# Optimization experiments

Measured on AMD Instinct MI355X. Metric: run time of the kernel, lower is better.

The kernel has to match this reference:

```python
import jax, jax.numpy as jnp
import numpy as np

# Static graph structure: gene nodes first, GO-term nodes last (mask is sorted).
N_GENE, N_GOID = 40000, 10000
N = N_GENE + N_GOID
E = 800000
INPUT_DIM, H1, H2, OUT_DIM, GOID_DIM = 1280, 256, 128, 64, 4096


def setup_inputs() -> dict:
    key = jax.random.key(0)
    ks = jax.random.split(key, 16)
    s = 0.02
    return {
        "x": jax.random.normal(ks[0], (N, GOID_DIM), jnp.float32),
        "edge_index": jax.random.randint(ks[1], (2, E), 0, N),
        "mask": jnp.concatenate([jnp.ones(N_GENE, bool), jnp.zeros(N_GOID, bool)]),
        # goid_dnn: Linear(4096,1024) -> ReLU -> Linear(1024,INPUT_DIM) -> ReLU
        "Wd1": jax.random.normal(ks[2], (GOID_DIM, 1024), jnp.float32) * s,
        "bd1": jnp.zeros((1024,), jnp.float32),
        "Wd2": jax.random.normal(ks[3], (1024, INPUT_DIM), jnp.float32) * s,
        "bd2": jnp.zeros((INPUT_DIM,), jnp.float32),
        # GCNConv layers
        "W1": jax.random.normal(ks[4], (INPUT_DIM, H1), jnp.float32) * s,
        "b1": jnp.zeros((H1,), jnp.float32),
        "W2": jax.random.normal(ks[5], (H1, H2), jnp.float32) * s,
        "b2": jnp.zeros((H2,), jnp.float32),
        # goid projections
        "Wp1": jax.random.normal(ks[6], (INPUT_DIM, H1), jnp.float32) * s,
        "bp1": jnp.zeros((H1,), jnp.float32),
        "Wp2": jax.random.normal(ks[7], (H1, H2), jnp.float32) * s,
        "bp2": jnp.zeros((H2,), jnp.float32),
        # final fc
        "Wf": jax.random.normal(ks[8], (H2, OUT_DIM), jnp.float32) * s,
        "bf": jnp.zeros((OUT_DIM,), jnp.float32),
    }


def gcn_conv(x, W, b, src, dst):
    """PyG GCNConv: xW, then sym-normalized (A + I) aggregation, then bias."""
    # degree over targets with self-loops already appended to (src, dst)
    deg = jax.ops.segment_sum(jnp.ones_like(dst, x.dtype), dst, num_segments=N)
    dinv = jnp.where(deg > 0, jax.lax.rsqrt(deg), 0.0)
    norm = dinv[src] * dinv[dst]                       # [E+N]
    xw = x @ W                                          # [N, F_out]
    msg = xw[src] * norm[:, None]                       # gather-scale, [E+N, F_out]
    return jax.ops.segment_sum(msg, dst, num_segments=N) + b


def reference(x, edge_index, mask, Wd1, bd1, Wd2, bd2, W1, b1, W2, b2,
              Wp1, bp1, Wp2, bp2, Wf, bf):
    del mask  # structurally: first N_GENE rows are genes, rest are GO terms
    loop = jnp.arange(N, dtype=edge_index.dtype)
    src = jnp.concatenate([edge_index[0], loop])
    dst = jnp.concatenate([edge_index[1], loop])

    gene_x = x[:N_GENE, :INPUT_DIM]
    goid_x = x[N_GENE:]
    # goid_dnn runs under torch.no_grad() -> stop_gradient
    goid_t = jax.lax.stop_gradient(
        jax.nn.relu(jax.nn.relu(goid_x @ Wd1 + bd1) @ Wd2 + bd2))

    x_t = jnp.concatenate([gene_x, goid_t], axis=0)      # [N, INPUT_DIM]
    h1 = jax.nn.relu(gcn_conv(x_t, W1, b1, src, dst))    # dropout disabled (eval)
    p1 = goid_t @ Wp1 + bp1                              # goid_proj1
    h1 = h1.at[N_GENE:].set(p1)                          # masked scatter assign
    h2 = jax.nn.relu(gcn_conv(h1, W2, b2, src, dst))
    h2 = h2.at[N_GENE:].set(p1 @ Wp2 + bp2)              # goid_proj2(goid_proj1(...))
    return h2 @ Wf + bf                                  # [N, OUT_DIM]
```

## Files before the change

kernel.cpp:

```cpp
#include <hip/hip_runtime.h>

constexpr int kNGene = 40000;
constexpr int kNGoid = 10000;
constexpr int kN     = 50000;
constexpr int kE     = 800000;
constexpr int kInDim = 1280;
constexpr int kH1    = 256;
constexpr int kH2    = 128;
constexpr int kOut   = 64;
constexpr int kGDim  = 4096;
constexpr int kD1    = 1024;

typedef short bf16x8 __attribute__((ext_vector_type(8)));
typedef float f32x4  __attribute__((ext_vector_type(4)));

static __device__ __forceinline__ short f2bf(float f) {
  union { float f; unsigned u; } v; v.f = f;
  unsigned r = v.u + 0x7FFF + ((v.u >> 16) & 1);
  return (short)(r >> 16);
}
static __device__ __forceinline__ float bf2f(short s) {
  union { unsigned u; float f; } v;
  v.u = ((unsigned)(unsigned short)s) << 16;
  return v.f;
}
static __device__ __forceinline__ void gld16(const void* g, void* l) {
  __builtin_amdgcn_global_load_lds(
      (const __attribute__((address_space(1))) void*)g,
      (__attribute__((address_space(3))) void*)l, 16, 0, 0);
}

__global__ __launch_bounds__(256)
void k_cvt_rows(const float* __restrict__ src, int lda, short* __restrict__ dst,
                int rows, int cols) {
  int chunks_per_row = cols >> 3;
  long long total = (long long)rows * chunks_per_row;
  long long stride = (long long)gridDim.x * blockDim.x;
  for (long long i = blockIdx.x * (long long)blockDim.x + threadIdx.x; i < total; i += stride) {
    int r = (int)(i / chunks_per_row);
    int c = (int)(i - (long long)r * chunks_per_row) << 3;
    const float* sp = src + (size_t)r * lda + c;
    float4 v0 = *reinterpret_cast<const float4*>(sp);
    float4 v1 = *reinterpret_cast<const float4*>(sp + 4);
    bf16x8 t;
    t[0]=f2bf(v0.x); t[1]=f2bf(v0.y); t[2]=f2bf(v0.z); t[3]=f2bf(v0.w);
    t[4]=f2bf(v1.x); t[5]=f2bf(v1.y); t[6]=f2bf(v1.z); t[7]=f2bf(v1.w);
    *reinterpret_cast<bf16x8*>(dst + (size_t)r * cols + c) = t;
  }
}

__global__ void k_init(float* deg, int* gcount) {
  int i = blockIdx.x * blockDim.x + threadIdx.x;
  if (i < kN) deg[i] = 1.0f;
  if (i == 0) *gcount = 0;
}
__global__ void k_deg_hist(const int* __restrict__ ei, float* __restrict__ deg) {
  int e = blockIdx.x * blockDim.x + threadIdx.x;
  if (e < kE) atomicAdd(&deg[ei[kE + e]], 1.0f);
}
__global__ void k_rowassign(const float* __restrict__ deg, int* __restrict__ rowstart,
                            int* __restrict__ cursor, int* __restrict__ gcount) {
  int i = blockIdx.x * blockDim.x + threadIdx.x;
  int lane = threadIdx.x & 63;
  int c = (i < kNGene) ? ((int)deg[i] - 1) : 0;
  int incl = c;
#pragma unroll
  for (int off = 1; off < 64; off <<= 1) {
    int t = __shfl_up(incl, off, 64);
    if (lane >= off) incl += t;
  }
  int total = __shfl(incl, 63, 64);
  int base = 0;
  if (lane == 63) base = atomicAdd(gcount, total);
  base = __shfl(base, 63, 64);
  if (i < kNGene) {
    int s = base + incl - c;
    rowstart[i] = s;
    cursor[i] = s;
  }
}
__global__ void k_fill(const int* __restrict__ ei, const float* __restrict__ deg,
                       int* __restrict__ cursor, int2* __restrict__ edges) {
  int e = blockIdx.x * blockDim.x + threadIdx.x;
  if (e >= kE) return;
  int dst = ei[kE + e];
  if (dst >= kNGene) return;
  int src = ei[e];
  int pos = atomicAdd(&cursor[dst], 1);
  float nrm = rsqrtf(deg[src] * deg[dst]);
  edges[pos] = make_int2(src, __float_as_int(nrm));
}

template <int F, int OBF>
__global__ __launch_bounds__(256)
void k_gather_bf(const short* __restrict__ xw, const float* __restrict__ deg,
                 const int* __restrict__ rowstart, const int2* __restrict__ edges,
                 const float* __restrict__ bias, void* __restrict__ hv) {
  constexpr int VEC = F / 64;
  int row = (blockIdx.x * blockDim.x + threadIdx.x) >> 6;
  int lane = threadIdx.x & 63;
  if (row >= kNGene) return;
  float dg = deg[row];
  float inv = 1.0f / dg;
  float acc[VEC];
  {
    const short* xr = xw + (size_t)row * F + lane * VEC;
    if constexpr (VEC == 4) {
      short4 s = *reinterpret_cast<const short4*>(xr);
      acc[0] = bf2f(s.x) * inv; acc[1] = bf2f(s.y) * inv;
      acc[2] = bf2f(s.z) * inv; acc[3] = bf2f(s.w) * inv;
    } else {
      short2 s = *reinterpret_cast<const short2*>(xr);
      acc[0] = bf2f(s.x) * inv; acc[1] = bf2f(s.y) * inv;
    }
  }
  const int2* ep = edges + rowstart[row];
  int n = (int)dg - 1;
  int e = 0;
  for (; e + 1 < n; e += 2) {
    int2 p0 = ep[e], p1 = ep[e + 1];
    float n0 = __int_as_float(p0.y), n1 = __int_as_float(p1.y);
    const short* x0 = xw + (size_t)p0.x * F + lane * VEC;
    const short* x1 = xw + (size_t)p1.x * F + lane * VEC;
    if constexpr (VEC == 4) {
      short4 s0 = *reinterpret_cast<const short4*>(x0);
      short4 s1 = *reinterpret_cast<const short4*>(x1);
      acc[0] += bf2f(s0.x) * n0; acc[1] += bf2f(s0.y) * n0;
      acc[2] += bf2f(s0.z) * n0; acc[3] += bf2f(s0.w) * n0;
      acc[0] += bf2f(s1.x) * n1; acc[1] += bf2f(s1.y) * n1;
      acc[2] += bf2f(s1.z) * n1; acc[3] += bf2f(s1.w) * n1;
    } else {
      short2 s0 = *reinterpret_cast<const short2*>(x0);
      short2 s1 = *reinterpret_cast<const short2*>(x1);
      acc[0] += bf2f(s0.x) * n0; acc[1] += bf2f(s0.y) * n0;
      acc[0] += bf2f(s1.x) * n1; acc[1] += bf2f(s1.y) * n1;
    }
  }
  if (e < n) {
    int2 p0 = ep[e];
    float n0 = __int_as_float(p0.y);
    const short* x0 = xw + (size_t)p0.x * F + lane * VEC;
    if constexpr (VEC == 4) {
      short4 s0 = *reinterpret_cast<const short4*>(x0);
      acc[0] += bf2f(s0.x) * n0; acc[1] += bf2f(s0.y) * n0;
      acc[2] += bf2f(s0.z) * n0; acc[3] += bf2f(s0.w) * n0;
    } else {
      short2 s0 = *reinterpret_cast<const short2*>(x0);
      acc[0] += bf2f(s0.x) * n0; acc[1] += bf2f(s0.y) * n0;
    }
  }
#pragma unroll
  for (int v = 0; v < VEC; ++v) acc[v] = fmaxf(acc[v] + bias[lane * VEC + v], 0.f);
  if constexpr (OBF) {
    short* hp = (short*)hv + (size_t)row * F + lane * VEC;
    if constexpr (VEC == 4) {
      short4 o; o.x = f2bf(acc[0]); o.y = f2bf(acc[1]); o.z = f2bf(acc[2]); o.w = f2bf(acc[3]);
      *reinterpret_cast<short4*>(hp) = o;
    } else {
      short2 o; o.x = f2bf(acc[0]); o.y = f2bf(acc[1]);
      *reinterpret_cast<short2*>(hp) = o;
    }
  } else {
    float* hp = (float*)hv + (size_t)row * F + lane * VEC;
    if constexpr (VEC == 4) {
      float4 o; o.x = acc[0]; o.y = acc[1]; o.z = acc[2]; o.w = acc[3];
      *reinterpret_cast<float4*>(hp) = o;
    } else {
      float2 o; o.x = acc[0]; o.y = acc[1];
      *reinterpret_cast<float2*>(hp) = o;
    }
  }
}

__global__ __launch_bounds__(256)
void k_wtrans_all(const float* __restrict__ Wd1, short* __restrict__ Wd1t,
                  const float* __restrict__ Wd2, short* __restrict__ Wd2t,
                  const float* __restrict__ W1,  short* __restrict__ W1t,
                  const float* __restrict__ Wp1, short* __restrict__ Wp1t,
                  const float* __restrict__ W2,  short* __restrict__ W2t,
                  const float* __restrict__ Wp2, short* __restrict__ Wp2t) {
  __shared__ float t[32][33];
  int b = blockIdx.x;
  const float* W; short* Wt; int K, N, bi;
  if (b < 4096)      { W = Wd1; Wt = Wd1t; K = 4096; N = 1024; bi = b; }
  else if (b < 5376) { W = Wd2; Wt = Wd2t; K = 1024; N = 1280; bi = b - 4096; }
  else if (b < 5696) { W = W1;  Wt = W1t;  K = 1280; N = 256;  bi = b - 5376; }
  else if (b < 6016) { W = Wp1; Wt = Wp1t; K = 1280; N = 256;  bi = b - 5696; }
  else if (b < 6048) { W = W2;  Wt = W2t;  K = 256;  N = 128;  bi = b - 6016; }
  else               { W = Wp2; Wt = Wp2t; K = 256;  N = 128;  bi = b - 6048; }
  int nbx = N >> 5;
  int n0 = (bi % nbx) * 32, k0 = (bi / nbx) * 32;
  int tx = threadIdx.x & 31, ty = threadIdx.x >> 5;
#pragma unroll
  for (int p = 0; p < 4; ++p)
    t[ty + 8 * p][tx] = W[(size_t)(k0 + ty + 8 * p) * N + n0 + tx];
  __syncthreads();
#pragma unroll
  for (int p = 0; p < 4; ++p)
    Wt[(size_t)(n0 + ty + 8 * p) * K + k0 + tx] = f2bf(t[tx][ty + 8 * p]);
}

template <int RELU, int OBF>
__global__ __launch_bounds__(256)
void k_gemm_bf16a(const short* __restrict__ A, int lda,
                  const short* __restrict__ Bt,
                  const float* __restrict__ bias,
                  void* __restrict__ Cv, int ldc,
                  int M, int K)
{
  __shared__ __align__(16) short As[2][128 * 32];
  __shared__ __align__(16) short Bs[2][128 * 32];
  const int tid  = threadIdx.x;
  const int lane = tid & 63;
  const int wid  = tid >> 6;
  const int wr = wid >> 1, wc = wid & 1;
  const int row0 = blockIdx.y * 128;
  const int col0 = blockIdx.x * 128;
  const int l15 = lane & 15, l4 = lane >> 4;
  const int srow = lane >> 2, schunk = lane & 3;

  f32x4 acc[4][4] = {};

  auto stage = [&](int buf, int k0) {
#pragma unroll
    for (int q = 0; q < 2; ++q) {
      int seg = wid * 2 + q;
      int r = seg * 16 + srow;
      int grow = row0 + r;
      if (grow >= M) grow = M - 1;
      gld16(A + (size_t)grow * lda + k0 + schunk * 8, &As[buf][seg * 512]);
      int gcol = col0 + r;
      gld16(Bt + (size_t)gcol * K + k0 + schunk * 8, &Bs[buf][seg * 512]);
    }
  };

  stage(0, 0);
  __syncthreads();
  int cur = 0;
  for (int k0 = 0; k0 < K; k0 += 32) {
    if (k0 + 32 < K) stage(cur ^ 1, k0 + 32);
    bf16x8 af[4], bfr[4];
#pragma unroll
    for (int m = 0; m < 4; ++m)
      af[m] = *reinterpret_cast<bf16x8*>(&As[cur][(wr * 64 + m * 16 + l15) * 32 + l4 * 8]);
#pragma unroll
    for (int n = 0; n < 4; ++n)
      bfr[n] = *reinterpret_cast<bf16x8*>(&Bs[cur][(wc * 64 + n * 16 + l15) * 32 + l4 * 8]);
#pragma unroll
    for (int m = 0; m < 4; ++m)
#pragma unroll
      for (int n = 0; n < 4; ++n)
        acc[m][n] = __builtin_amdgcn_mfma_f32_16x16x32_bf16(af[m], bfr[n], acc[m][n], 0, 0, 0);
    __syncthreads();
    cur ^= 1;
  }

#pragma unroll
  for (int n = 0; n < 4; ++n) {
    int col = col0 + wc * 64 + n * 16 + l15;
    float bv = bias ? bias[col] : 0.f;
#pragma unroll
    for (int m = 0; m < 4; ++m) {
      int rb = row0 + wr * 64 + m * 16 + l4 * 4;
#pragma unroll
      for (int e = 0; e < 4; ++e) {
        int r = rb + e;
        if (r < M) {
          float v = acc[m][n][e] + bv;
          if (RELU) v = fmaxf(v, 0.f);
          size_t idx = (size_t)r * ldc + col;
          if constexpr (OBF) ((short*)Cv)[idx] = f2bf(v);
          else               ((float*)Cv)[idx] = v;
        }
      }
    }
  }
}

template <int RELU, int OBF>
__global__ __launch_bounds__(512)
void k_gemm_wide(const short* __restrict__ A, int lda,
                 const short* __restrict__ Bt,
                 const float* __restrict__ bias,
                 void* __restrict__ Cv, int ldc,
                 int M, int K)
{
  __shared__ __align__(16) short As[2][128 * 32];
  __shared__ __align__(16) short Bs[2][256 * 32];
  const int tid  = threadIdx.x;
  const int lane = tid & 63;
  const int wid  = tid >> 6;
  const int wr = wid >> 2, wc = wid & 3;
  int nwg = gridDim.x * gridDim.y;
  int b0 = blockIdx.y * gridDim.x + blockIdx.x;
  int qq = nwg >> 3, rr = nwg & 7, xcd = b0 & 7, j = b0 >> 3;
  int swz = ((xcd < rr) ? xcd * (qq + 1) : rr * (qq + 1) + (xcd - rr) * qq) + j;
  const int row0 = (swz / gridDim.x) * 128;
  const int col0 = (swz % gridDim.x) * 256;
  const int l15 = lane & 15, l4 = lane >> 4;
  const int srow = lane >> 2, schunk = lane & 3;

  f32x4 acc[4][4] = {};

  auto stage = [&](int buf, int k0) {
#pragma unroll
    for (int q = 0; q < 3; ++q) {
      int s = wid * 3 + q;
      if (s < 8) {
        int grow = row0 + s * 16 + srow;
        if (grow >= M) grow = M - 1;
        gld16(A + (size_t)grow * lda + k0 + schunk * 8, &As[buf][s * 512]);
      } else {
        int gcol = col0 + (s - 8) * 16 + srow;
        gld16(Bt + (size_t)gcol * K + k0 + schunk * 8, &Bs[buf][(s - 8) * 512]);
      }
    }
  };

  stage(0, 0);
  __syncthreads();
  int cur = 0;
  for (int k0 = 0; k0 < K; k0 += 32) {
    if (k0 + 32 < K) stage(cur ^ 1, k0 + 32);
    bf16x8 af[4], bfr[4];
#pragma unroll
    for (int m = 0; m < 4; ++m)
      af[m] = *reinterpret_cast<bf16x8*>(&As[cur][(wr * 64 + m * 16 + l15) * 32 + l4 * 8]);
#pragma unroll
    for (int n = 0; n < 4; ++n)
      bfr[n] = *reinterpret_cast<bf16x8*>(&Bs[cur][(wc * 64 + n * 16 + l15) * 32 + l4 * 8]);
#pragma unroll
    for (int m = 0; m < 4; ++m)
#pragma unroll
      for (int n = 0; n < 4; ++n)
        acc[m][n] = __builtin_amdgcn_mfma_f32_16x16x32_bf16(af[m], bfr[n], acc[m][n], 0, 0, 0);
    __syncthreads();
    cur ^= 1;
  }

#pragma unroll
  for (int n = 0; n < 4; ++n) {
    int col = col0 + wc * 64 + n * 16 + l15;
    float bv = bias ? bias[col] : 0.f;
#pragma unroll
    for (int m = 0; m < 4; ++m) {
      int rb = row0 + wr * 64 + m * 16 + l4 * 4;
#pragma unroll
      for (int e = 0; e < 4; ++e) {
        int r = rb + e;
        if (r < M) {
          float v = acc[m][n][e] + bv;
          if (RELU) v = fmaxf(v, 0.f);
          size_t idx = (size_t)r * ldc + col;
          if constexpr (OBF) ((short*)Cv)[idx] = f2bf(v);
          else               ((float*)Cv)[idx] = v;
        }
      }
    }
  }
}

__global__ __launch_bounds__(512)
void k_combo_wide(const short* __restrict__ A, int lda,
                  const short* __restrict__ Bt,
                  const float* __restrict__ bp1,
                  short* __restrict__ X1, short* __restrict__ H1,
                  int M, int K)
{
  __shared__ __align__(16) short As[2][128 * 32];
  __shared__ __align__(16) short Bs[2][256 * 32];
  const int tid  = threadIdx.x;
  const int lane = tid & 63;
  const int wid  = tid >> 6;
  const int wr = wid >> 2, wc = wid & 3;
  const int row0 = blockIdx.y * 128;
  const int col0 = blockIdx.x * 256;
  const int l15 = lane & 15, l4 = lane >> 4;
  const int srow = lane >> 2, schunk = lane & 3;

  f32x4 acc[4][4] = {};

  auto stage = [&](int buf, int k0) {
#pragma unroll
    for (int q = 0; q < 3; ++q) {
      int s = wid * 3 + q;
      if (s < 8) {
        int grow = row0 + s * 16 + srow;
        if (grow >= M) grow = M - 1;
        gld16(A + (size_t)grow * lda + k0 + schunk * 8, &As[buf][s * 512]);
      } else {
        int gcol = col0 + (s - 8) * 16 + srow;
        gld16(Bt + (size_t)gcol * K + k0 + schunk * 8, &Bs[buf][(s - 8) * 512]);
      }
    }
  };

  stage(0, 0);
  __syncthreads();
  int cur = 0;
  for (int k0 = 0; k0 < K; k0 += 32) {
    if (k0 + 32 < K) stage(cur ^ 1, k0 + 32);
    bf16x8 af[4], bfr[4];
#pragma unroll
    for (int m = 0; m < 4; ++m)
      af[m] = *reinterpret_cast<bf16x8*>(&As[cur][(wr * 64 + m * 16 + l15) * 32 + l4 * 8]);
#pragma unroll
    for (int n = 0; n < 4; ++n)
      bfr[n] = *reinterpret_cast<bf16x8*>(&Bs[cur][(wc * 64 + n * 16 + l15) * 32 + l4 * 8]);
#pragma unroll
    for (int m = 0; m < 4; ++m)
#pragma unroll
      for (int n = 0; n < 4; ++n)
        acc[m][n] = __builtin_amdgcn_mfma_f32_16x16x32_bf16(af[m], bfr[n], acc[m][n], 0, 0, 0);
    __syncthreads();
    cur ^= 1;
  }

  const int is_p1 = (col0 >= 256);
  short* dstp = is_p1 ? H1 : X1;
#pragma unroll
  for (int n = 0; n < 4; ++n) {
    int cl = wc * 64 + n * 16 + l15;
    float bv = is_p1 ? bp1[cl] : 0.f;
#pragma unroll
    for (int m = 0; m < 4; ++m) {
      int rb = row0 + wr * 64 + m * 16 + l4 * 4;
#pragma unroll
      for (int e = 0; e < 4; ++e) {
        int r = rb + e;
        if (r < M) dstp[(size_t)r * 256 + cl] = f2bf(acc[m][n][e] + bv);
      }
    }
  }
}

__global__ __launch_bounds__(512)
void k_gemm_gene(const float* __restrict__ A, int lda,
                 const short* __restrict__ Bt,
                 short* __restrict__ C,
                 int M, int K)
{
  __shared__ short As[2][128 * 40];
  __shared__ __align__(16) short Bs[2][256 * 32];
  const int tid  = threadIdx.x;
  const int lane = tid & 63;
  const int wid  = tid >> 6;
  const int wr = wid >> 2, wc = wid & 3;
  const int row0 = blockIdx.x * 128;
  const int l15 = lane & 15, l4 = lane >> 4;
  const int sr = tid >> 2, sc = tid & 3;
  const int srow = lane >> 2, schunk = lane & 3;

  f32x4 acc[4][4] = {};

  auto stageB = [&](int buf, int k0) {
#pragma unroll
    for (int q = 0; q < 2; ++q) {
      int seg = wid * 2 + q;
      int gcol = seg * 16 + srow;
      gld16(Bt + (size_t)gcol * K + k0 + schunk * 8, &Bs[buf][seg * 512]);
    }
  };
  auto stageA = [&](int buf, int k0) {
    int grow = row0 + sr;
    float4 v0 = make_float4(0.f,0.f,0.f,0.f), v1 = v0;
    if (grow < M) {
      const float* ap = A + (size_t)grow * lda + k0 + sc * 8;
      v0 = *reinterpret_cast<const float4*>(ap);
      v1 = *reinterpret_cast<const float4*>(ap + 4);
    }
    bf16x8 t;
    t[0]=f2bf(v0.x); t[1]=f2bf(v0.y); t[2]=f2bf(v0.z); t[3]=f2bf(v0.w);
    t[4]=f2bf(v1.x); t[5]=f2bf(v1.y); t[6]=f2bf(v1.z); t[7]=f2bf(v1.w);
    *reinterpret_cast<bf16x8*>(&As[buf][sr * 40 + sc * 8]) = t;
  };

  stageB(0, 0); stageA(0, 0);
  __syncthreads();
  int cur = 0;
  for (int k0 = 0; k0 < K; k0 += 32) {
    if (k0 + 32 < K) { stageB(cur ^ 1, k0 + 32); stageA(cur ^ 1, k0 + 32); }
    bf16x8 af[4], bfr[4];
#pragma unroll
    for (int m = 0; m < 4; ++m)
      af[m] = *reinterpret_cast<bf16x8*>(&As[cur][(wr * 64 + m * 16 + l15) * 40 + l4 * 8]);
#pragma unroll
    for (int n = 0; n < 4; ++n)
      bfr[n] = *reinterpret_cast<bf16x8*>(&Bs[cur][(wc * 64 + n * 16 + l15) * 32 + l4 * 8]);
#pragma unroll
    for (int m = 0; m < 4; ++m)
#pragma unroll
      for (int n = 0; n < 4; ++n)
        acc[m][n] = __builtin_amdgcn_mfma_f32_16x16x32_bf16(af[m], bfr[n], acc[m][n], 0, 0, 0);
    __syncthreads();
    cur ^= 1;
  }

#pragma unroll
  for (int n = 0; n < 4; ++n) {
    int col = wc * 64 + n * 16 + l15;
#pragma unroll
    for (int m = 0; m < 4; ++m) {
      int rb = row0 + wr * 64 + m * 16 + l4 * 4;
#pragma unroll
      for (int e = 0; e < 4; ++e) {
        int r = rb + e;
        if (r < M) C[(size_t)r * 256 + col] = f2bf(acc[m][n][e]);
      }
    }
  }
}

__global__ __launch_bounds__(256)
void k_gemm_f32(const float* __restrict__ A, int lda,
                const float* __restrict__ B, int ldb,
                const float* __restrict__ bias,
                float* __restrict__ C, int ldc,
                int M, int Ncol, int K, int do_relu)
{
  __shared__ float As[16][65];
  __shared__ float Bs[16][68];
  const int tid = threadIdx.x;
  const int tx = tid & 15, ty = tid >> 4;
  const int row0 = blockIdx.y * 64;
  const int col0 = blockIdx.x * 64;
  float acc[4][4] = {};
  for (int k0 = 0; k0 < K; k0 += 16) {
    {
      int r = tid >> 2;
      int c = (tid & 3) << 2;
      int grow = row0 + r;
      float4 v = make_float4(0.f, 0.f, 0.f, 0.f);
      if (grow < M)
        v = *reinterpret_cast<const float4*>(A + (size_t)grow * lda + k0 + c);
      As[c + 0][r] = v.x; As[c + 1][r] = v.y; As[c + 2][r] = v.z; As[c + 3][r] = v.w;
    }
    {
      int r = tid >> 4;
      int c = (tid & 15) << 2;
      int gcol = col0 + c;
      float4 v = make_float4(0.f, 0.f, 0.f, 0.f);
      if (gcol < Ncol)
        v = *reinterpret_cast<const float4*>(B + (size_t)(k0 + r) * ldb + gcol);
      *reinterpret_cast<float4*>(&Bs[r][c]) = v;
    }
    __syncthreads();
#pragma unroll
    for (int k = 0; k < 16; ++k) {
      float a[4], b[4];
#pragma unroll
      for (int i = 0; i < 4; ++i) a[i] = As[k][ty + 16 * i];
#pragma unroll
      for (int j = 0; j < 4; ++j) b[j] = Bs[k][tx + 16 * j];
#pragma unroll
      for (int i = 0; i < 4; ++i)
#pragma unroll
        for (int j = 0; j < 4; ++j)
          acc[i][j] = fmaf(a[i], b[j], acc[i][j]);
    }
    __syncthreads();
  }
#pragma unroll
  for (int i = 0; i < 4; ++i) {
    int r = row0 + ty + 16 * i;
    if (r >= M) continue;
#pragma unroll
    for (int j = 0; j < 4; ++j) {
      int ccol = col0 + tx + 16 * j;
      if (ccol >= Ncol) continue;
      float v = acc[i][j];
      if (bias) v += bias[ccol];
      if (do_relu) v = fmaxf(v, 0.f);
      C[(size_t)r * ldc + ccol] = v;
    }
  }
}

extern "C" void kernel_launch(void* const* d_in, const int* in_sizes, int n_in,
                              void* d_out, int out_size, void* d_ws, size_t ws_size,
                              hipStream_t stream) {
  const float* x   = (const float*)d_in[0];
  const int*   ei  = (const int*)d_in[1];
  const float* Wd1 = (const float*)d_in[3];
  const float* bd1 = (const float*)d_in[4];
  const float* Wd2 = (const float*)d_in[5];
  const float* bd2 = (const float*)d_in[6];
  const float* W1  = (const float*)d_in[7];
  const float* b1  = (const float*)d_in[8];
  const float* W2  = (const float*)d_in[9];
  const float* b2  = (const float*)d_in[10];
  const float* Wp1 = (const float*)d_in[11];
  const float* bp1 = (const float*)d_in[12];
  const float* Wp2 = (const float*)d_in[13];
  const float* bp2 = (const float*)d_in[14];
  const float* Wf  = (const float*)d_in[15];
  const float* bf_ = (const float*)d_in[16];
  float* out = (float*)d_out;
  float* ws  = (float*)d_ws;

  short* goidx_bf = (short*)(ws + 0);
  short* goidt_bf = (short*)(ws + 20480000);
  short* h1tmp_bf = (short*)(ws + 26880000);
  short* Wd1t = (short*)(ws + 32000000);
  short* Wd2t = (short*)(ws + 34097152);
  short* W1t  = (short*)(ws + 34752512);
  short* Wp1t = (short*)(ws + 34916352);
  short* W2t  = (short*)(ws + 35080192);
  short* xw1_bf = (short*)(ws + 35100000);
  short* h1bf   = (short*)(ws + 41500000);
  short* xw2_bf = (short*)(ws + 50460000);
  float* h2     = ws + 53660000;
  float* deg    = ws + 60060000;
  int*   rowstart = (int*)(ws + 60150016);
  int*   cursor   = (int*)(ws + 60190016);
  int2*  edges    = (int2*)(ws + 60230016);
  int*   gcount   = (int*)(ws + 61830016);
  short* Wp2t = (short*)(ws + 61830032);

  const float* gene_x = x;
  const float* goid_x = x + (size_t)kNGene * kGDim;

  auto gb = [](int M, int Ncol) { return dim3((unsigned)(Ncol / 128), (unsigned)((M + 127) / 128)); };
  auto gw = [](int M, int Ncol) { return dim3((unsigned)(Ncol / 256), (unsigned)((M + 127) / 128)); };
  auto gf = [](int M, int Ncol) { return dim3((unsigned)((Ncol + 63) / 64), (unsigned)((M + 63) / 64)); };

  k_cvt_rows<<<2048, 256, 0, stream>>>(goid_x, kGDim, goidx_bf, kNGoid, kGDim);
  k_wtrans_all<<<6080, 256, 0, stream>>>(Wd1, Wd1t, Wd2, Wd2t, W1, W1t,
                                         Wp1, Wp1t, W2, W2t, Wp2, Wp2t);

  k_init<<<(kN + 255) / 256, 256, 0, stream>>>(deg, gcount);
  k_deg_hist<<<(kE + 255) / 256, 256, 0, stream>>>(ei, deg);
  k_rowassign<<<(kNGene + 255) / 256, 256, 0, stream>>>(deg, rowstart, cursor, gcount);
  k_fill<<<(kE + 255) / 256, 256, 0, stream>>>(ei, deg, cursor, edges);

  k_gemm_wide<1,1><<<gw(kNGoid, kD1), 512, 0, stream>>>(goidx_bf, kGDim, Wd1t, bd1,
                                                        h1tmp_bf, kD1, kNGoid, kGDim);
  k_gemm_wide<1,1><<<gw(kNGoid, kInDim), 512, 0, stream>>>(h1tmp_bf, kD1, Wd2t, bd2,
                                                           goidt_bf, kInDim, kNGoid, kD1);

  k_gemm_gene<<<dim3((kNGene + 127) / 128), 512, 0, stream>>>(gene_x, kGDim, W1t,
                                                              xw1_bf, kNGene, kInDim);

  k_combo_wide<<<dim3(2, (kNGoid + 127) / 128), 512, 0, stream>>>(
      goidt_bf, kInDim, W1t , bp1,
      xw1_bf + (size_t)kNGene * kH1, h1bf + (size_t)kNGene * kH1,
      kNGoid, kInDim);

  k_gather_bf<kH1,1><<<(kNGene * 64 + 255) / 256, 256, 0, stream>>>(
      xw1_bf, deg, rowstart, edges, b1, h1bf);

  k_gemm_bf16a<0,1><<<gb(kN, kH2), 256, 0, stream>>>(h1bf, kH1, W2t, nullptr,
                                                     xw2_bf, kH2, kN, kH1);

  k_gather_bf<kH2,0><<<(kNGene * 64 + 255) / 256, 256, 0, stream>>>(
      xw2_bf, deg, rowstart, edges, b2, h2);
  k_gemm_bf16a<0,0><<<gb(kNGoid, kH2), 256, 0, stream>>>(
      h1bf + (size_t)kNGene * kH1, kH1, Wp2t, bp2,
      h2 + (size_t)kNGene * kH2, kH2, kNGoid, kH1);

  k_gemm_f32<<<gf(kN, kOut), 256, 0, stream>>>(h2, kH2, Wf, kOut, bf_, out, kOut,
                                               kN, kOut, kH2, 0);
}
```

Baseline: 610.6 us.

## Merge prep kernels, triple-buffer GEMM loads, and use bf16 MFMA for output GEMM

Folds the goid conversion, weight transposes (now including Wf) and degree init into a single prep launch, which cuts launch overhead. The bf16 GEMMs switch from double to triple buffering, using explicit vmcnt waits so two tiles are in flight at once. h2 is now stored in bf16, and the final fp32 FMA GEMM is replaced by an MFMA bf16 kernel. This lowers output precision and uses more LDS per block, which may reduce occupancy.

```diff
diff --git a/kernel.cpp b/kernel.cpp
--- a/kernel.cpp
+++ b/kernel.cpp
@@ -29,31 +29,72 @@
       (const __attribute__((address_space(1))) void*)g,
       (__attribute__((address_space(3))) void*)l, 16, 0, 0);
 }
+template <int N>
+static __device__ __forceinline__ void wait_barrier() {
+  if constexpr (N == 0)      asm volatile("s_waitcnt vmcnt(0)" ::: "memory");
+  else if constexpr (N == 3) asm volatile("s_waitcnt vmcnt(3)" ::: "memory");
+  else                       asm volatile("s_waitcnt vmcnt(4)" ::: "memory");
+  __builtin_amdgcn_s_barrier();
+  asm volatile("" ::: "memory");
+}
+
+constexpr int kCvtBlocks   = 20000;
+constexpr int kTransBlocks = 6088;
+constexpr int kInitBlocks  = 196;
 
 __global__ __launch_bounds__(256)
-void k_cvt_rows(const float* __restrict__ src, int lda, short* __restrict__ dst,
-                int rows, int cols) {
-  int chunks_per_row = cols >> 3;
-  long long total = (long long)rows * chunks_per_row;
-  long long stride = (long long)gridDim.x * blockDim.x;
-  for (long long i = blockIdx.x * (long long)blockDim.x + threadIdx.x; i < total; i += stride) {
-    int r = (int)(i / chunks_per_row);
-    int c = (int)(i - (long long)r * chunks_per_row) << 3;
-    const float* sp = src + (size_t)r * lda + c;
+void k_prep(const float* __restrict__ goid_x, short* __restrict__ goidx_bf,
+            const float* __restrict__ Wd1, short* __restrict__ Wd1t,
+            const float* __restrict__ Wd2, short* __restrict__ Wd2t,
+            const float* __restrict__ W1,  short* __restrict__ W1t,
+            const float* __restrict__ Wp1, short* __restrict__ Wp1t,
+            const float* __restrict__ W2,  short* __restrict__ W2t,
+            const float* __restrict__ Wp2, short* __restrict__ Wp2t,
+            const float* __restrict__ Wf,  short* __restrict__ Wft,
+            float* __restrict__ deg, int* __restrict__ gcount)
+{
+  __shared__ float t[32][33];
+  int b = blockIdx.x;
+  if (b < kCvtBlocks) {
+    int idx = b * 256 + threadIdx.x;
+    int r = idx >> 9;
+    int c = (idx & 511) << 3;
+    const float* sp = goid_x + (size_t)r * kGDim + c;
     float4 v0 = *reinterpret_cast<const float4*>(sp);
     float4 v1 = *reinterpret_cast<const float4*>(sp + 4);
-    bf16x8 t;
-    t[0]=f2bf(v0.x); t[1]=f2bf(v0.y); t[2]=f2bf(v0.z); t[3]=f2bf(v0.w);
-    t[4]=f2bf(v1.x); t[5]=f2bf(v1.y); t[6]=f2bf(v1.z); t[7]=f2bf(v1.w);
-    *reinterpret_cast<bf16x8*>(dst + (size_t)r * cols + c) = t;
-  }
-}
-
-__global__ void k_init(float* deg, int* gcount) {
-  int i = blockIdx.x * blockDim.x + threadIdx.x;
-  if (i < kN) deg[i] = 1.0f;
-  if (i == 0) *gcount = 0;
-}
+    bf16x8 o;
+    o[0]=f2bf(v0.x); o[1]=f2bf(v0.y); o[2]=f2bf(v0.z); o[3]=f2bf(v0.w);
+    o[4]=f2bf(v1.x); o[5]=f2bf(v1.y); o[6]=f2bf(v1.z); o[7]=f2bf(v1.w);
+    *reinterpret_cast<bf16x8*>(goidx_bf + (size_t)r * kGDim + c) = o;
+    return;
+  }
+  if (b >= kCvtBlocks + kTransBlocks) {
+    int i = (b - kCvtBlocks - kTransBlocks) * 256 + threadIdx.x;
+    if (i < kN) deg[i] = 1.0f;
+    if (i == 0) *gcount = 0;
+    return;
+  }
+  int b2 = b - kCvtBlocks;
+  const float* W; short* Wt; int K, N, bi;
+  if (b2 < 4096)      { W = Wd1; Wt = Wd1t; K = 4096; N = 1024; bi = b2; }
+  else if (b2 < 5376) { W = Wd2; Wt = Wd2t; K = 1024; N = 1280; bi = b2 - 4096; }
+  else if (b2 < 5696) { W = W1;  Wt = W1t;  K = 1280; N = 256;  bi = b2 - 5376; }
+  else if (b2 < 6016) { W = Wp1; Wt = Wp1t; K = 1280; N = 256;  bi = b2 - 5696; }
+  else if (b2 < 6048) { W = W2;  Wt = W2t;  K = 256;  N = 128;  bi = b2 - 6016; }
+  else if (b2 < 6080) { W = Wp2; Wt = Wp2t; K = 256;  N = 128;  bi = b2 - 6048; }
+  else                { W = Wf;  Wt = Wft;  K = 128;  N = 64;   bi = b2 - 6080; }
+  int nbx = N >> 5;
+  int n0 = (bi % nbx) * 32, k0 = (bi / nbx) * 32;
+  int tx = threadIdx.x & 31, ty = threadIdx.x >> 5;
+#pragma unroll
+  for (int p = 0; p < 4; ++p)
+    t[ty + 8 * p][tx] = W[(size_t)(k0 + ty + 8 * p) * N + n0 + tx];
+  __syncthreads();
+#pragma unroll
+  for (int p = 0; p < 4; ++p)
+    Wt[(size_t)(n0 + ty + 8 * p) * K + k0 + tx] = f2bf(t[tx][ty + 8 * p]);
+}
+
 __global__ void k_deg_hist(const int* __restrict__ ei, float* __restrict__ deg) {
   int e = blockIdx.x * blockDim.x + threadIdx.x;
   if (e < kE) atomicAdd(&deg[ei[kE + e]], 1.0f);
@@ -172,34 +213,6 @@
   }
 }
 
-__global__ __launch_bounds__(256)
-void k_wtrans_all(const float* __restrict__ Wd1, short* __restrict__ Wd1t,
-                  const float* __restrict__ Wd2, short* __restrict__ Wd2t,
-                  const float* __restrict__ W1,  short* __restrict__ W1t,
-                  const float* __restrict__ Wp1, short* __restrict__ Wp1t,
-                  const float* __restrict__ W2,  short* __restrict__ W2t,
-                  const float* __restrict__ Wp2, short* __restrict__ Wp2t) {
-  __shared__ float t[32][33];
-  int b = blockIdx.x;
-  const float* W; short* Wt; int K, N, bi;
-  if (b < 4096)      { W = Wd1; Wt = Wd1t; K = 4096; N = 1024; bi = b; }
-  else if (b < 5376) { W = Wd2; Wt = Wd2t; K = 1024; N = 1280; bi = b - 4096; }
-  else if (b < 5696) { W = W1;  Wt = W1t;  K = 1280; N = 256;  bi = b - 5376; }
-  else if (b < 6016) { W = Wp1; Wt = Wp1t; K = 1280; N = 256;  bi = b - 5696; }
-  else if (b < 6048) { W = W2;  Wt = W2t;  K = 256;  N = 128;  bi = b - 6016; }
-  else               { W = Wp2; Wt = Wp2t; K = 256;  N = 128;  bi = b - 6048; }
-  int nbx = N >> 5;
-  int n0 = (bi % nbx) * 32, k0 = (bi / nbx) * 32;
-  int tx = threadIdx.x & 31, ty = threadIdx.x >> 5;
-#pragma unroll
-  for (int p = 0; p < 4; ++p)
-    t[ty + 8 * p][tx] = W[(size_t)(k0 + ty + 8 * p) * N + n0 + tx];
-  __syncthreads();
-#pragma unroll
-  for (int p = 0; p < 4; ++p)
-    Wt[(size_t)(n0 + ty + 8 * p) * K + k0 + tx] = f2bf(t[tx][ty + 8 * p]);
-}
-
 template <int RELU, int OBF>
 __global__ __launch_bounds__(256)
 void k_gemm_bf16a(const short* __restrict__ A, int lda,
@@ -208,8 +221,8 @@
                   void* __restrict__ Cv, int ldc,
                   int M, int K)
 {
-  __shared__ __align__(16) short As[2][128 * 32];
-  __shared__ __align__(16) short Bs[2][128 * 32];
+  __shared__ __align__(16) short As[3][128 * 32];
+  __shared__ __align__(16) short Bs[3][128 * 32];
   const int tid  = threadIdx.x;
   const int lane = tid & 63;
   const int wid  = tid >> 6;
@@ -234,11 +247,14 @@
     }
   };
 
+  const int nt = K >> 5;
   stage(0, 0);
-  __syncthreads();
-  int cur = 0;
-  for (int k0 = 0; k0 < K; k0 += 32) {
-    if (k0 + 32 < K) stage(cur ^ 1, k0 + 32);
+  if (nt > 1) { stage(1, 32); wait_barrier<4>(); }
+  else        { wait_barrier<0>(); }
+
+  for (int t = 0; t < nt; ++t) {
+    if (t + 2 < nt) stage((t + 2) % 3, (t + 2) * 32);
+    const int cur = t % 3;
     bf16x8 af[4], bfr[4];
 #pragma unroll
     for (int m = 0; m < 4; ++m)
@@ -251,8 +267,9 @@
 #pragma unroll
       for (int n = 0; n < 4; ++n)
         acc[m][n] = __builtin_amdgcn_mfma_f32_16x16x32_bf16(af[m], bfr[n], acc[m][n], 0, 0, 0);
-    __syncthreads();
-    cur ^= 1;
+    if (t + 1 < nt) {
+      if (t + 2 < nt) wait_barrier<4>(); else wait_barrier<0>();
+    }
   }
 
 #pragma unroll
@@ -285,8 +302,8 @@
                  void* __restrict__ Cv, int ldc,
                  int M, int K)
 {
-  __shared__ __align__(16) short As[2][128 * 32];
-  __shared__ __align__(16) short Bs[2][256 * 32];
+  __shared__ __align__(16) short As[3][128 * 32];
+  __shared__ __align__(16) short Bs[3][256 * 32];
   const int tid  = threadIdx.x;
   const int lane = tid & 63;
   const int wid  = tid >> 6;
@@ -317,11 +334,14 @@
     }
   };
 
+  const int nt = K >> 5;
   stage(0, 0);
-  __syncthreads();
-  int cur = 0;
-  for (int k0 = 0; k0 < K; k0 += 32) {
-    if (k0 + 32 < K) stage(cur ^ 1, k0 + 32);
+  if (nt > 1) { stage(1, 32); wait_barrier<3>(); }
+  else        { wait_barrier<0>(); }
+
+  for (int t = 0; t < nt; ++t) {
+    if (t + 2 < nt) stage((t + 2) % 3, (t + 2) * 32);
+    const int cur = t % 3;
     bf16x8 af[4], bfr[4];
 #pragma unroll
     for (int m = 0; m < 4; ++m)
@@ -334,8 +354,9 @@
 #pragma unroll
       for (int n = 0; n < 4; ++n)
         acc[m][n] = __builtin_amdgcn_mfma_f32_16x16x32_bf16(af[m], bfr[n], acc[m][n], 0, 0, 0);
-    __syncthreads();
-    cur ^= 1;
+    if (t + 1 < nt) {
+      if (t + 2 < nt) wait_barrier<3>(); else wait_barrier<0>();
+    }
   }
 
 #pragma unroll
@@ -512,66 +533,68 @@
 }
 
 __global__ __launch_bounds__(256)
-void k_gemm_f32(const float* __restrict__ A, int lda,
-                const float* __restrict__ B, int ldb,
+void k_gemm_out(const short* __restrict__ A,
+                const short* __restrict__ Bt,
                 const float* __restrict__ bias,
-                float* __restrict__ C, int ldc,
-                int M, int Ncol, int K, int do_relu)
+                float* __restrict__ C,
+                int M)
 {
-  __shared__ float As[16][65];
-  __shared__ float Bs[16][68];
-  const int tid = threadIdx.x;
-  const int tx = tid & 15, ty = tid >> 4;
-  const int row0 = blockIdx.y * 64;
-  const int col0 = blockIdx.x * 64;
-  float acc[4][4] = {};
-  for (int k0 = 0; k0 < K; k0 += 16) {
-    {
-      int r = tid >> 2;
-      int c = (tid & 3) << 2;
-      int grow = row0 + r;
-      float4 v = make_float4(0.f, 0.f, 0.f, 0.f);
-      if (grow < M)
-        v = *reinterpret_cast<const float4*>(A + (size_t)grow * lda + k0 + c);
-      As[c + 0][r] = v.x; As[c + 1][r] = v.y; As[c + 2][r] = v.z; As[c + 3][r] = v.w;
-    }
-    {
-      int r = tid >> 4;
-      int c = (tid & 15) << 2;
-      int gcol = col0 + c;
-      float4 v = make_float4(0.f, 0.f, 0.f, 0.f);
-      if (gcol < Ncol)
-        v = *reinterpret_cast<const float4*>(B + (size_t)(k0 + r) * ldb + gcol);
-      *reinterpret_cast<float4*>(&Bs[r][c]) = v;
-    }
+  __shared__ __align__(16) short As[2][256 * 32];
+  __shared__ __align__(16) short Bs[2][64 * 32];
+  const int tid  = threadIdx.x;
+  const int lane = tid & 63;
+  const int wid  = tid >> 6;
+  const int row0 = blockIdx.x * 256;
+  const int l15 = lane & 15, l4 = lane >> 4;
+  const int srow = lane >> 2, schunk = lane & 3;
+
+  f32x4 acc[4][4] = {};
+
+  auto stage = [&](int buf, int k0) {
+#pragma unroll
+    for (int q = 0; q < 4; ++q) {
+      int seg = wid * 4 + q;
+      int grow = row0 + seg * 16 + srow;
+      if (grow >= M) grow = M - 1;
+      gld16(A + (size_t)grow * 128 + k0 + schunk * 8, &As[buf][seg * 512]);
+    }
+    int gcol = wid * 16 + srow;
+    gld16(Bt + (size_t)gcol * 128 + k0 + schunk * 8, &Bs[buf][wid * 512]);
+  };
+
+  stage(0, 0);
+  __syncthreads();
+  int cur = 0;
+  for (int k0 = 0; k0 < 128; k0 += 32) {
+    if (k0 + 32 < 128) stage(cur ^ 1, k0 + 32);
+    bf16x8 af[4], bfr[4];
+#pragma unroll
+    for (int m = 0; m < 4; ++m)
+      af[m] = *reinterpret_cast<bf16x8*>(&As[cur][(wid * 64 + m * 16 + l15) * 32 + l4 * 8]);
+#pragma unroll
+    for (int n = 0; n < 4; ++n)
+      bfr[n] = *reinterpret_cast<bf16x8*>(&Bs[cur][(n * 16 + l15) * 32 + l4 * 8]);
+#pragma unroll
+    for (int m = 0; m < 4; ++m)
+#pragma unroll
+      for (int n = 0; n < 4; ++n)
+        acc[m][n] = __builtin_amdgcn_mfma_f32_16x16x32_bf16(af[m], bfr[n], acc[m][n], 0, 0, 0);
     __syncthreads();
-#pragma unroll
-    for (int k = 0; k < 16; ++k) {
-      float a[4], b[4];
-#pragma unroll
-      for (int i = 0; i < 4; ++i) a[i] = As[k][ty + 16 * i];
-#pragma unroll
-      for (int j = 0; j < 4; ++j) b[j] = Bs[k][tx + 16 * j];
-#pragma unroll
-      for (int i = 0; i < 4; ++i)
-#pragma unroll
-        for (int j = 0; j < 4; ++j)
-          acc[i][j] = fmaf(a[i], b[j], acc[i][j]);
-    }
-    __syncthreads();
-  }
-#pragma unroll
-  for (int i = 0; i < 4; ++i) {
-    int r = row0 + ty + 16 * i;
-    if (r >= M) continue;
-#pragma unroll
-    for (int j = 0; j < 4; ++j) {
-      int ccol = col0 + tx + 16 * j;
-      if (ccol >= Ncol) continue;
-      float v = acc[i][j];
-      if (bias) v += bias[ccol];
-      if (do_relu) v = fmaxf(v, 0.f);
-      C[(size_t)r * ldc + ccol] = v;
+    cur ^= 1;
+  }
+
+#pragma unroll
+  for (int n = 0; n < 4; ++n) {
+    int col = n * 16 + l15;
+    float bv = bias[col];
+#pragma unroll
+    for (int m = 0; m < 4; ++m) {
+      int rb = row0 + wid * 64 + m * 16 + l4 * 4;
+#pragma unroll
+      for (int e = 0; e < 4; ++e) {
+        int r = rb + e;
+        if (r < M) C[(size_t)r * 64 + col] = acc[m][n][e] + bv;
+      }
     }
   }
 }
@@ -609,26 +632,25 @@
   short* xw1_bf = (short*)(ws + 35100000);
   short* h1bf   = (short*)(ws + 41500000);
   short* xw2_bf = (short*)(ws + 50460000);
-  float* h2     = ws + 53660000;
+  short* h2bf   = (short*)(ws + 53660000);
   float* deg    = ws + 60060000;
   int*   rowstart = (int*)(ws + 60150016);
   int*   cursor   = (int*)(ws + 60190016);
   int2*  edges    = (int2*)(ws + 60230016);
   int*   gcount   = (int*)(ws + 61830016);
   short* Wp2t = (short*)(ws + 61830032);
+  short* Wft  = (short*)(ws + 61846416);
 
   const float* gene_x = x;
   const float* goid_x = x + (size_t)kNGene * kGDim;
 
   auto gb = [](int M, int Ncol) { return dim3((unsigned)(Ncol / 128), (unsigned)((M + 127) / 128)); };
   auto gw = [](int M, int Ncol) { return dim3((unsigned)(Ncol / 256), (unsigned)((M + 127) / 128)); };
-  auto gf = [](int M, int Ncol) { return dim3((unsigned)((Ncol + 63) / 64), (unsigned)((M + 63) / 64)); };
-
-  k_cvt_rows<<<2048, 256, 0, stream>>>(goid_x, kGDim, goidx_bf, kNGoid, kGDim);
-  k_wtrans_all<<<6080, 256, 0, stream>>>(Wd1, Wd1t, Wd2, Wd2t, W1, W1t,
-                                         Wp1, Wp1t, W2, W2t, Wp2, Wp2t);
-
-  k_init<<<(kN + 255) / 256, 256, 0, stream>>>(deg, gcount);
+
+  k_prep<<<kCvtBlocks + kTransBlocks + kInitBlocks, 256, 0, stream>>>(
+      goid_x, goidx_bf, Wd1, Wd1t, Wd2, Wd2t, W1, W1t, Wp1, Wp1t,
+      W2, W2t, Wp2, Wp2t, Wf, Wft, deg, gcount);
+
   k_deg_hist<<<(kE + 255) / 256, 256, 0, stream>>>(ei, deg);
   k_rowassign<<<(kNGene + 255) / 256, 256, 0, stream>>>(deg, rowstart, cursor, gcount);
   k_fill<<<(kE + 255) / 256, 256, 0, stream>>>(ei, deg, cursor, edges);
@@ -652,12 +674,11 @@
   k_gemm_bf16a<0,1><<<gb(kN, kH2), 256, 0, stream>>>(h1bf, kH1, W2t, nullptr,
                                                      xw2_bf, kH2, kN, kH1);
 
-  k_gather_bf<kH2,0><<<(kNGene * 64 + 255) / 256, 256, 0, stream>>>(
-      xw2_bf, deg, rowstart, edges, b2, h2);
-  k_gemm_bf16a<0,0><<<gb(kNGoid, kH2), 256, 0, stream>>>(
+  k_gather_bf<kH2,1><<<(kNGene * 64 + 255) / 256, 256, 0, stream>>>(
+      xw2_bf, deg, rowstart, edges, b2, h2bf);
+  k_gemm_bf16a<0,1><<<gb(kNGoid, kH2), 256, 0, stream>>>(
       h1bf + (size_t)kNGene * kH1, kH1, Wp2t, bp2,
-      h2 + (size_t)kNGene * kH2, kH2, kNGoid, kH1);
-
-  k_gemm_f32<<<gf(kN, kOut), 256, 0, stream>>>(h2, kH2, Wf, kOut, bf_, out, kOut,
-                                               kN, kOut, kH2, 0);
-}
+      h2bf + (size_t)kNGene * kH2, kH2, kNGoid, kH1);
+
+  k_gemm_out<<<(kN + 255) / 256, 256, 0, stream>>>(h2bf, Wft, bf_, out, kN);
+}
```

After: 609.3 us. Within noise of the previous version (-0.2%).
